# Performance work log

Measured on AMD Instinct MI355X. Metric: run time of the kernel, lower is better.

## Reference

```python
import jax, jax.numpy as jnp
import numpy as np

SEQ, BATCH = 1024, 2
N_HEAD, D_MODEL = 16, 1024
Q_LORA, KV_LORA = 20, 20
ROPE = D_MODEL // N_HEAD // 2   # 32 qk_rope_head_dim
NOPE = D_MODEL // N_HEAD // 2   # 32 qk_nope_head_dim
V_DIM = D_MODEL // N_HEAD       # 64
N_EXP, HID = 4, 1024            # hidden_dim = d_inner//5 = 5120//5
N_GROUP, TOPK_GROUP, TOP_K = 2, 2, 1
ROUTED_SCALE = 1.0


def setup_inputs() -> dict:
    key = jax.random.key(0)
    ks = jax.random.split(key, 16)
    sc = 0.02
    return {
        'dec_inp': jax.random.normal(ks[0], (SEQ, BATCH, D_MODEL), jnp.float32),
        'wq_a': jax.random.normal(ks[1], (D_MODEL, Q_LORA), jnp.float32) * sc,
        'q_norm_w': jnp.ones((Q_LORA,), jnp.float32),
        'wq_b': jax.random.normal(ks[2], (Q_LORA, N_HEAD * (NOPE + ROPE)), jnp.float32) * sc,
        'wkv_a': jax.random.normal(ks[3], (D_MODEL, KV_LORA + ROPE), jnp.float32) * sc,
        'kv_norm_w': jnp.ones((KV_LORA,), jnp.float32),
        'wkv_b': jax.random.normal(ks[4], (KV_LORA, N_HEAD * (NOPE + V_DIM)), jnp.float32) * sc,
        'wo': jax.random.normal(ks[5], (N_HEAD * V_DIM, D_MODEL), jnp.float32) * sc,
        'gate_w': jax.random.normal(ks[6], (N_EXP, D_MODEL), jnp.float32) * sc,
        'exp_gate': jax.random.normal(ks[7], (N_EXP, D_MODEL, HID), jnp.float32) * sc,
        'exp_up': jax.random.normal(ks[8], (N_EXP, D_MODEL, HID), jnp.float32) * sc,
        'exp_down': jax.random.normal(ks[9], (N_EXP, HID, D_MODEL), jnp.float32) * sc,
        'sh_gate': jax.random.normal(ks[10], (D_MODEL, HID), jnp.float32) * sc,
        'sh_up': jax.random.normal(ks[11], (D_MODEL, HID), jnp.float32) * sc,
        'sh_down': jax.random.normal(ks[12], (HID, D_MODEL), jnp.float32) * sc,
    }


def _rms(x, w, eps=1e-6):
    return x * jax.lax.rsqrt(jnp.mean(x * x, axis=-1, keepdims=True) + eps) * w


def _freqs(seqlen):
    # precompute_freqs_cis(rope_dim * n_head, seqlen): dim = 512 here
    dim = ROPE * N_HEAD
    inv = 1.0 / (10000.0 ** (jnp.arange(0, dim, 2, dtype=jnp.float32) / dim))  # [dim//2]
    ang = jnp.arange(seqlen, dtype=jnp.float32)[:, None] * inv[None, :]       # [s, dim//2]
    ang = ang.reshape(seqlen, N_HEAD, ROPE // 2)
    return jnp.cos(ang), jnp.sin(ang)


def _rope(x, cos, sin):
    # x: [b, s, h, ROPE]; interleaved-pair complex rotation
    b, s, h, _ = x.shape
    xr = x.reshape(b, s, h, ROPE // 2, 2)
    x0, x1 = xr[..., 0], xr[..., 1]
    c = cos[None]  # [1, s, h, ROPE//2]
    sn = sin[None]
    o0 = x0 * c - x1 * sn
    o1 = x0 * sn + x1 * c
    return jnp.stack([o0, o1], axis=-1).reshape(b, s, h, ROPE)


def reference(dec_inp, wq_a, q_norm_w, wq_b, wkv_a, kv_norm_w, wkv_b, wo,
              gate_w, exp_gate, exp_up, exp_down, sh_gate, sh_up, sh_down):
    x = jnp.swapaxes(dec_inp, 0, 1)  # [b, s, d]
    b, s, d = x.shape
    # ---- MLA attention ----
    q = _rms(x @ wq_a, q_norm_w) @ wq_b                       # [b, s, h*(nope+rope)]
    q = q.reshape(b, s, N_HEAD, NOPE + ROPE)
    q_nope, q_pe = q[..., :NOPE], q[..., NOPE:]
    kv = x @ wkv_a                                            # [b, s, kv_lora+rope]
    ckv, k_pe = kv[..., :KV_LORA], kv[..., KV_LORA:]
    kvb = (_rms(ckv, kv_norm_w) @ wkv_b).reshape(b, s, N_HEAD, NOPE + V_DIM)
    k_nope, v = kvb[..., :NOPE], kvb[..., NOPE:]
    cos, sin = _freqs(s)
    q_pe = _rope(q_pe, cos, sin)
    k_pe_h = _rope(jnp.broadcast_to(k_pe[:, :, None, :], (b, s, N_HEAD, ROPE)), cos, sin)
    qf = jnp.concatenate([q_nope, q_pe], axis=-1)             # [b, s, h, 64]
    kf = jnp.concatenate([k_nope, k_pe_h], axis=-1)
    scale = 1.0 / np.sqrt(NOPE + ROPE)
    scores = jnp.einsum('bshd,bthd->bhst', qf, kf) * scale    # mask=None in the source forward
    probs = jax.nn.softmax(scores, axis=-1)
    attn = jnp.einsum('bhst,bthd->bshd', probs, v).reshape(b, s, N_HEAD * V_DIM)
    y = attn @ wo                                             # [b, s, d]
    y = jnp.swapaxes(y, 0, 1)                                 # [s, b, d]
    # ---- DeepSeekMoE (group_limited_greedy, top_k=1, 1 shared expert) ----
    xf = y.reshape(-1, d)                                     # [T, d]
    T = xf.shape[0]
    sc = jax.nn.softmax(xf @ gate_w.T, axis=-1)               # [T, E]
    gsc = sc.reshape(T, N_GROUP, N_EXP // N_GROUP).max(axis=-1)  # [T, n_group]
    _, gidx = jax.lax.top_k(gsc, TOPK_GROUP)
    gmask = jax.nn.one_hot(gidx, N_GROUP, dtype=sc.dtype).sum(axis=1)  # [T, n_group]
    smask = jnp.repeat(gmask, N_EXP // N_GROUP, axis=-1)      # [T, E]
    tw, ti = jax.lax.top_k(jnp.where(smask > 0, sc, 0.0), TOP_K)
    comb = (jax.nn.one_hot(ti, N_EXP, dtype=sc.dtype) * tw[..., None]).sum(axis=1) * ROUTED_SCALE  # [T, E]
    g = jnp.einsum('td,edh->teh', xf, exp_gate)
    u = jnp.einsum('td,edh->teh', xf, exp_up)
    dn = jnp.einsum('teh,ehd->ted', jax.nn.silu(g) * u, exp_down)
    routed = jnp.einsum('ted,te->td', dn, comb)
    shared = (jax.nn.silu(xf @ sh_gate) * (xf @ sh_up)) @ sh_down
    return (routed + shared).reshape(s, b, d)
```

## Files before the change

### kernel.cpp

```cpp
#include <hip/hip_runtime.h>
#include <hip/hip_bf16.h>
#include <math.h>

#define SEQ 1024
#define BATCH 2
#define T 2048
#define DM 1024
#define NH 16
#define NOPE 32
#define HD 64
#define QL 20
#define KVL 20
#define KVA 52
#define HID 1024
#define NEXP 4
#define LSTR 80

typedef short bf16x8 __attribute__((ext_vector_type(8)));
typedef float f32x4 __attribute__((ext_vector_type(4)));
typedef float f32x16 __attribute__((ext_vector_type(16)));
typedef __hip_bfloat16 bf16;

static __device__ __forceinline__ float sigmoidf_(float x) {
    return 1.0f / (1.0f + __expf(-x));
}
static __device__ __forceinline__ unsigned short bfbits(float x) {
    bf16 h = __float2bfloat16(x);
    return *reinterpret_cast<unsigned short*>(&h);
}
static __device__ __forceinline__ unsigned cvt_pk_bf16(float lo, float hi) {
    unsigned r;
    asm("v_cvt_pk_bf16_f32 %0, %1, %2" : "=v"(r) : "v"(lo), "v"(hi));
    return r;
}
static __device__ __forceinline__ void gload16(const bf16* g, char* l) {
    __builtin_amdgcn_global_load_lds(
        (const __attribute__((address_space(1))) unsigned int*)g,
        (__attribute__((address_space(3))) unsigned int*)l, 16, 0, 0);
}
static __device__ __forceinline__ void barrier_() {
    asm volatile("" ::: "memory");
    __builtin_amdgcn_s_barrier();
    asm volatile("" ::: "memory");
}
#define VMWAIT(N) asm volatile("s_waitcnt vmcnt(" #N ")" ::: "memory")

__global__ __launch_bounds__(256) void k_setup(
    const float* __restrict__ wo, const float* __restrict__ sg,
    const float* __restrict__ su, const float* __restrict__ sd,
    const float* __restrict__ eg, const float* __restrict__ eu,
    const float* __restrict__ ed,
    bf16* __restrict__ woT, bf16* __restrict__ sgT, bf16* __restrict__ suT,
    bf16* __restrict__ sdT, bf16* __restrict__ egT, bf16* __restrict__ euT,
    bf16* __restrict__ edT,
    const float* __restrict__ wq_a, const float* __restrict__ wkv_a,
    const float* __restrict__ wq_b, const float* __restrict__ wkv_b,
    bf16* __restrict__ loraT, bf16* __restrict__ wqbT, bf16* __restrict__ wkvbT,
    float* __restrict__ ctab, float* __restrict__ stab)
{
    int z = blockIdx.z;
    int tid = threadIdx.x;
    if (z < 16) {
        __shared__ float tile[32][33];
        const float* in; bf16* out;
        if      (z == 0) { in = wo; out = woT; }
        else if (z == 1) { in = sg; out = sgT; }
        else if (z == 2) { in = su; out = suT; }
        else if (z == 3) { in = sd; out = sdT; }
        else if (z < 8)  { size_t o = (size_t)(z - 4)  * DM * HID; in = eg + o; out = egT + o; }
        else if (z < 12) { size_t o = (size_t)(z - 8)  * DM * HID; in = eu + o; out = euT + o; }
        else             { size_t o = (size_t)(z - 12) * HID * DM; in = ed + o; out = edT + o; }
        int c0 = blockIdx.x * 32, r0 = blockIdx.y * 32;
        int tx = tid & 31, ty = tid >> 5;
        #pragma unroll
        for (int ii = 0; ii < 4; ++ii)
            tile[ty + ii * 8][tx] = in[(size_t)(r0 + ty + ii * 8) * 1024 + c0 + tx];
        __syncthreads();
        int c = tid >> 3, rg = (tid & 7) * 4;
        ushort4 o4;
        o4.x = bfbits(tile[rg + 0][c]);
        o4.y = bfbits(tile[rg + 1][c]);
        o4.z = bfbits(tile[rg + 2][c]);
        o4.w = bfbits(tile[rg + 3][c]);
        *(ushort4*)&out[(size_t)(c0 + c) * 1024 + r0 + rg] = o4;
    } else if (z == 16) {
        int s = blockIdx.y * 32 + blockIdx.x;
        int p = tid;
        float freq = exp2f(-(float)p * (13.287712379549449f / 256.0f));
        float ang = (float)s * freq;
        float sn, cs;
        __sincosf(ang, &sn, &cs);
        ctab[s * 256 + p] = cs;
        stab[s * 256 + p] = sn;
    } else {
        int idx = (blockIdx.y * 32 + blockIdx.x) * 256 + tid;
        if (z == 17) {
            if (idx >= 80 * 1024) return;
            int n = idx >> 10, k = idx & 1023;
            float v = (n < 20) ? wq_a[k * QL + n] : (n < 72 ? wkv_a[k * KVA + (n - 20)] : 0.f);
            loraT[idx] = __float2bfloat16(v);
        } else if (z == 18) {
            if (idx >= 1024 * 32) return;
            int n = idx >> 5, k = idx & 31;
            wqbT[idx] = __float2bfloat16(k < 20 ? wq_b[k * DM + n] : 0.f);
        } else {
            if (idx >= 1536 * 32) return;
            int n = idx >> 5, k = idx & 31;
            wkvbT[idx] = __float2bfloat16(k < 20 ? wkv_b[k * (NH * 96) + n] : 0.f);
        }
    }
}

__global__ __launch_bounds__(256) void k_p1(
    const float* __restrict__ dec, const bf16* __restrict__ loraT,
    float* __restrict__ lora4)
{
    __shared__ __align__(16) char As[128 * LSTR];
    __shared__ __align__(16) char Bs[80 * LSTR];
    const int tid = threadIdx.x;
    const int kz = blockIdx.x;
    const int m0 = blockIdx.y * 128;
    const int lane = tid & 63, wave = tid >> 6;
    const int g = lane >> 4, c = lane & 15;
    f32x4 acc[2][5] = {};
    for (int ks = 0; ks < 16; ++ks) {
        int k0 = kz * 512 + ks * 32;
        __syncthreads();
        #pragma unroll
        for (int pass = 0; pass < 4; ++pass) {
            int row = (tid >> 3) + pass * 32;
            int t = m0 + row;
            int b = t >> 10, s = t & 1023;
            f32x4 v = *(const f32x4*)&dec[(size_t)(s * 2 + b) * DM + k0 + (tid & 7) * 4];
            ushort4 h4;
            h4.x = bfbits(v[0]); h4.y = bfbits(v[1]);
            h4.z = bfbits(v[2]); h4.w = bfbits(v[3]);
            *(ushort4*)&As[row * LSTR + (tid & 7) * 8] = h4;
        }
        if (tid < 160) {
            int row = tid >> 1, hf = tid & 1;
            const bf16* src = &loraT[row * 1024 + k0 + hf * 16];
            *(int4*)&Bs[row * LSTR + hf * 32]      = *(const int4*)&src[0];
            *(int4*)&Bs[row * LSTR + hf * 32 + 16] = *(const int4*)&src[8];
        }
        __syncthreads();
        bf16x8 af[2], bff[5];
        #pragma unroll
        for (int mi = 0; mi < 2; ++mi)
            af[mi] = *(const bf16x8*)&As[(wave * 32 + mi * 16 + c) * LSTR + 16 * g];
        #pragma unroll
        for (int nf = 0; nf < 5; ++nf)
            bff[nf] = *(const bf16x8*)&Bs[(nf * 16 + c) * LSTR + 16 * g];
        #pragma unroll
        for (int mi = 0; mi < 2; ++mi)
            #pragma unroll
            for (int nf = 0; nf < 5; ++nf)
                acc[mi][nf] = __builtin_amdgcn_mfma_f32_16x16x32_bf16(af[mi], bff[nf], acc[mi][nf], 0, 0, 0);
    }
    #pragma unroll
    for (int mi = 0; mi < 2; ++mi)
        #pragma unroll
        for (int nf = 0; nf < 5; ++nf)
            #pragma unroll
            for (int r = 0; r < 4; ++r) {
                int col = nf * 16 + c;
                if (col < 72) {
                    int row = m0 + wave * 32 + mi * 16 + 4 * g + r;
                    lora4[((size_t)kz * T + row) * 72 + col] = acc[mi][nf][r];
                }
            }
}

__global__ __launch_bounds__(256) void k_p2(
    const float* __restrict__ lora4, const float* __restrict__ qnw,
    const float* __restrict__ kvnw, bf16* __restrict__ nrmq, bf16* __restrict__ nrmkv,
    int* __restrict__ cnt)
{
    if (blockIdx.x == 0 && threadIdx.x < 16) cnt[threadIdx.x] = 0;
    int t = blockIdx.x * 256 + threadIdx.x;
    float lq[20], lk[20];
    float ssq = 0.f, ssk = 0.f;
    #pragma unroll
    for (int i = 0; i < 20; ++i) {
        lq[i] = lora4[t * 72 + i] + lora4[(size_t)(T + t) * 72 + i];
        ssq += lq[i] * lq[i];
    }
    #pragma unroll
    for (int i = 0; i < 20; ++i) {
        lk[i] = lora4[t * 72 + 20 + i] + lora4[(size_t)(T + t) * 72 + 20 + i];
        ssk += lk[i] * lk[i];
    }
    float fq = rsqrtf(ssq / 20.f + 1e-6f);
    float fk = rsqrtf(ssk / 20.f + 1e-6f);
    #pragma unroll
    for (int i = 0; i < 32; ++i) {
        nrmq[t * 32 + i]  = __float2bfloat16(i < 20 ? lq[i] * fq * qnw[i]  : 0.f);
        nrmkv[t * 32 + i] = __float2bfloat16(i < 20 ? lk[i] * fk * kvnw[i] : 0.f);
    }
}

__global__ __launch_bounds__(256) void k_p2b(
    const float* __restrict__ lora4, const float* __restrict__ ctab,
    const float* __restrict__ stab, bf16* __restrict__ kb)
{
    int t = blockIdx.x, p = threadIdx.x;
    int r = p & 15, h = p >> 4, s = t & (SEQ - 1);
    float y0 = lora4[t * 72 + 40 + 2 * r] + lora4[(size_t)(T + t) * 72 + 40 + 2 * r];
    float y1 = lora4[t * 72 + 41 + 2 * r] + lora4[(size_t)(T + t) * 72 + 41 + 2 * r];
    float cs = ctab[s * 256 + p], sn = stab[s * 256 + p];
    ushort2 pk;
    pk.x = bfbits(y0 * cs - y1 * sn);
    pk.y = bfbits(y0 * sn + y1 * cs);
    *(ushort2*)&kb[(size_t)t * DM + h * HD + NOPE + 2 * r] = pk;
}

__global__ __launch_bounds__(256) void k_p3q(
    const bf16* __restrict__ nrmq, const bf16* __restrict__ wqbT,
    const float* __restrict__ ctab, const float* __restrict__ stab,
    bf16* __restrict__ qb)
{
    __shared__ __align__(16) char As[128 * LSTR];
    __shared__ __align__(16) char Bs[64 * LSTR];
    const int tid = threadIdx.x;
    const int m0 = blockIdx.y * 128, n0 = blockIdx.x * 64;
    const int lane = tid & 63, wave = tid >> 6;
    const int g = lane >> 4, c = lane & 15;
    const int wm = wave >> 1, wn = wave & 1;
    {
        int row = tid >> 1, hf = tid & 1;
        const bf16* sa = &nrmq[(size_t)(m0 + row) * 32 + hf * 16];
        *(int4*)&As[row * LSTR + hf * 32]      = *(const int4*)&sa[0];
        *(int4*)&As[row * LSTR + hf * 32 + 16] = *(const int4*)&sa[8];
        int brow = tid >> 2;
        *(int4*)&Bs[brow * LSTR + (tid & 3) * 16] = *(const int4*)&wqbT[(size_t)(n0 + brow) * 32 + (tid & 3) * 8];
    }
    __syncthreads();
    f32x4 acc[4][2] = {};
    bf16x8 af[4], bfr[2];
    #pragma unroll
    for (int mi = 0; mi < 4; ++mi)
        af[mi] = *(const bf16x8*)&As[(wm * 64 + mi * 16 + c) * LSTR + 16 * g];
    #pragma unroll
    for (int ni = 0; ni < 2; ++ni)
        bfr[ni] = *(const bf16x8*)&Bs[(wn * 32 + ni * 16 + c) * LSTR + 16 * g];
    #pragma unroll
    for (int mi = 0; mi < 4; ++mi)
        #pragma unroll
        for (int ni = 0; ni < 2; ++ni) {
            acc[mi][ni] = __builtin_amdgcn_mfma_f32_16x16x32_bf16(af[mi], bfr[ni], acc[mi][ni], 0, 0, 0);
            #pragma unroll
            for (int r = 0; r < 4; ++r) acc[mi][ni][r] *= 0.18033688f;
        }

    #pragma unroll
    for (int mi = 0; mi < 4; ++mi)
        #pragma unroll
        for (int ni = 0; ni < 2; ++ni) {
            int n = n0 + wn * 32 + ni * 16 + c;
            int w = n & 63;
            if (w < 32) {
                #pragma unroll
                for (int r = 0; r < 4; ++r) {
                    int row = m0 + wm * 64 + mi * 16 + 4 * g + r;
                    qb[(size_t)row * DM + n] = __float2bfloat16(acc[mi][ni][r]);
                }
            } else {
                int h = n >> 6;
                int pidx = h * 16 + ((w - 32) >> 1);
                int odd = w & 1;
                #pragma unroll
                for (int r = 0; r < 4; ++r) {
                    int row = m0 + wm * 64 + mi * 16 + 4 * g + r;
                    int s = row & (SEQ - 1);
                    float own = acc[mi][ni][r];
                    float oth = __shfl_xor(own, 1);
                    float cs = ctab[s * 256 + pidx], sn = stab[s * 256 + pidx];
                    float o = odd ? (oth * sn + own * cs) : (own * cs - oth * sn);
                    qb[(size_t)row * DM + n] = __float2bfloat16(o);
                }
            }
        }
}

__global__ __launch_bounds__(256) void k_p3kv(
    const bf16* __restrict__ nrmkv, const bf16* __restrict__ wkvbT,
    bf16* __restrict__ kb, bf16* __restrict__ vt_g)
{
    __shared__ __align__(16) char As[128 * LSTR];
    __shared__ __align__(16) char Bs[64 * LSTR];
    const int tid = threadIdx.x;
    const int m0 = blockIdx.y * 128, n0 = blockIdx.x * 64;
    const int lane = tid & 63, wave = tid >> 6;
    const int g = lane >> 4, c = lane & 15;
    const int wm = wave >> 1, wn = wave & 1;
    {
        int row = tid >> 1, hf = tid & 1;
        const bf16* sa = &nrmkv[(size_t)(m0 + row) * 32 + hf * 16];
        *(int4*)&As[row * LSTR + hf * 32]      = *(const int4*)&sa[0];
        *(int4*)&As[row * LSTR + hf * 32 + 16] = *(const int4*)&sa[8];
        int brow = tid >> 2;
        *(int4*)&Bs[brow * LSTR + (tid & 3) * 16] = *(const int4*)&wkvbT[(size_t)(n0 + brow) * 32 + (tid & 3) * 8];
    }
    __syncthreads();
    f32x4 acc[4][2] = {};
    bf16x8 af[4], bfr[2];
    #pragma unroll
    for (int mi = 0; mi < 4; ++mi)
        af[mi] = *(const bf16x8*)&As[(wm * 64 + mi * 16 + c) * LSTR + 16 * g];
    #pragma unroll
    for (int ni = 0; ni < 2; ++ni)
        bfr[ni] = *(const bf16x8*)&Bs[(wn * 32 + ni * 16 + c) * LSTR + 16 * g];
    #pragma unroll
    for (int mi = 0; mi < 4; ++mi)
        #pragma unroll
        for (int ni = 0; ni < 2; ++ni)
            acc[mi][ni] = __builtin_amdgcn_mfma_f32_16x16x32_bf16(af[mi], bfr[ni], acc[mi][ni], 0, 0, 0);

    #pragma unroll
    for (int mi = 0; mi < 4; ++mi)
        #pragma unroll
        for (int ni = 0; ni < 2; ++ni) {
            int n = n0 + wn * 32 + ni * 16 + c;
            int h = n / 96, w = n - h * 96;
            int row0 = m0 + wm * 64 + mi * 16 + 4 * g;
            if (w < NOPE) {
                #pragma unroll
                for (int r = 0; r < 4; ++r)
                    kb[(size_t)(row0 + r) * DM + h * HD + w] = __float2bfloat16(acc[mi][ni][r]);
            } else {
                int d = w - NOPE;
                int b = row0 >> 10, s0 = row0 & (SEQ - 1);
                ushort4 v4;
                v4.x = bfbits(acc[mi][ni][0]);
                v4.y = bfbits(acc[mi][ni][1]);
                v4.z = bfbits(acc[mi][ni][2]);
                v4.w = bfbits(acc[mi][ni][3]);
                *(ushort4*)&vt_g[(((size_t)(b * NH + h) * HD + d) << 10) + s0] = v4;
            }
        }
}

__global__ __launch_bounds__(256) void k_attn(
    const bf16* __restrict__ qb, const bf16* __restrict__ kb,
    const bf16* __restrict__ vt_g, bf16* __restrict__ ab)
{
    __shared__ __align__(16) char stage[2][16384];
    __shared__ float pol[2][32][65];
    __shared__ float mll[2][32][2];

    const int qt = blockIdx.x, h = blockIdx.y, b = blockIdx.z;
    const int tid = threadIdx.x;
    const int lane = tid & 63, wave = tid >> 6;
    const int l31 = lane & 31, hi = lane >> 5;
    const int sp = wave >> 1, wq = wave & 1;
    const int q0 = qt * 64 + wq * 32;
    char* ks = stage[sp];
    char* vt = stage[sp] + 8192;
    const int ptid = tid & 127;

    bf16x8 qf[4];
    {
        const bf16* qrow = &qb[(size_t)(b * SEQ + q0 + l31) * DM + h * HD + 8 * hi];
        #pragma unroll
        for (int st = 0; st < 4; ++st)
            qf[st] = *(const bf16x8*)&qrow[16 * st];
    }

    f32x16 o0 = {}, o1 = {};
    float m_run = -3.0e38f, l_run = 0.f;
    const size_t vbase = ((size_t)(b * NH + h) * HD) << 10;

    for (int ktl = 0; ktl < 8; ++ktl) {
        const int kt = sp * 8 + ktl;
        __syncthreads();
        #pragma unroll
        for (int ps = 0; ps < 4; ++ps) {
            int row = (ptid >> 3) + ps * 16;
            int col8 = (ptid & 7) * 8;
            int sw = (col8 * 2) ^ ((row & 7) << 4);
            int4 kv4 = *(const int4*)&kb[(size_t)(b * SEQ + kt * 64 + row) * DM + h * HD + col8];
            *(int4*)&ks[row * 128 + sw] = kv4;
            int4 vv4 = *(const int4*)&vt_g[vbase + ((size_t)row << 10) + kt * 64 + col8];
            *(int4*)&vt[row * 128 + sw] = vv4;
        }
        __syncthreads();

        f32x16 sc0 = {}, sc1 = {};
        #pragma unroll
        for (int st = 0; st < 4; ++st) {
            int colb = 32 * st + 16 * hi;
            int r0 = l31;
            bf16x8 kf0 = *(const bf16x8*)&ks[r0 * 128 + (colb ^ ((r0 & 7) << 4))];
            sc0 = __builtin_amdgcn_mfma_f32_32x32x16_bf16(kf0, qf[st], sc0, 0, 0, 0);
            int r1 = 32 + l31;
            bf16x8 kf1 = *(const bf16x8*)&ks[r1 * 128 + (colb ^ ((r1 & 7) << 4))];
            sc1 = __builtin_amdgcn_mfma_f32_32x32x16_bf16(kf1, qf[st], sc1, 0, 0, 0);
        }

        float mt = fmaxf(sc0[0], sc1[0]);
        #pragma unroll
        for (int i = 1; i < 16; ++i) mt = fmaxf(mt, fmaxf(sc0[i], sc1[i]));
        mt = fmaxf(mt, __shfl_xor(mt, 32));

        if (!__all(mt <= m_run + 8.0f)) {
            float m_new = fmaxf(m_run, mt);
            float corr = exp2f(m_run - m_new);
            m_run = m_new;
            l_run *= corr;
            #pragma unroll
            for (int i = 0; i < 16; ++i) { o0[i] *= corr; o1[i] *= corr; }
        }
        float ls = 0.f;
        #pragma unroll
        for (int i = 0; i < 16; ++i) {
            sc0[i] = exp2f(sc0[i] - m_run);
            sc1[i] = exp2f(sc1[i] - m_run);
            ls += sc0[i] + sc1[i];
        }
        ls += __shfl_xor(ls, 32);
        l_run += ls;

        unsigned pk0[8], pk1[8];
        #pragma unroll
        for (int i = 0; i < 8; ++i) {
            pk0[i] = cvt_pk_bf16(sc0[2 * i], sc0[2 * i + 1]);
            pk1[i] = cvt_pk_bf16(sc1[2 * i], sc1[2 * i + 1]);
        }

#define PV_SUB(PK, KK)                                                          \
        {                                                                       \
            _Pragma("unroll")                                                   \
            for (int s = 0; s < 2; ++s) {                                       \
                unsigned sx = hi ? PK[4*s]   : PK[4*s+2];                       \
                unsigned rx = __shfl_xor(sx, 32);                               \
                unsigned sy = hi ? PK[4*s+1] : PK[4*s+3];                       \
                unsigned ry = __shfl_xor(sy, 32);                               \
                int4 bi;                                                        \
                bi.x = hi ? (int)rx : (int)PK[4*s];                             \
                bi.y = hi ? (int)ry : (int)PK[4*s+1];                           \
                bi.z = hi ? (int)PK[4*s+2] : (int)rx;                           \
                bi.w = hi ? (int)PK[4*s+3] : (int)ry;                           \
                bf16x8 bfr = *(bf16x8*)&bi;                                     \
                int cb = (KK) * 64 + 32 * s + 16 * hi;                          \
                {                                                               \
                    int vr = l31;                                               \
                    bf16x8 vf = *(const bf16x8*)&vt[vr * 128 + (cb ^ ((vr & 7) << 4))]; \
                    o0 = __builtin_amdgcn_mfma_f32_32x32x16_bf16(vf, bfr, o0, 0, 0, 0); \
                }                                                               \
                {                                                               \
                    int vr = 32 + l31;                                          \
                    bf16x8 vf = *(const bf16x8*)&vt[vr * 128 + (cb ^ ((vr & 7) << 4))]; \
                    o1 = __builtin_amdgcn_mfma_f32_32x32x16_bf16(vf, bfr, o1, 0, 0, 0); \
                }                                                               \
            }                                                                   \
        }
        PV_SUB(pk0, 0)
        PV_SUB(pk1, 1)
#undef PV_SUB
    }

    if (sp == 1) {
        #pragma unroll
        for (int i = 0; i < 16; ++i) {
            int d = (i & 3) + 8 * (i >> 2) + 4 * hi;
            pol[wq][l31][d]      = o0[i];
            pol[wq][l31][32 + d] = o1[i];
        }
        if (hi == 0) { mll[wq][l31][0] = m_run; mll[wq][l31][1] = l_run; }
    }
    __syncthreads();
    if (sp == 1) return;

    float m_b = mll[wq][l31][0], l_b = mll[wq][l31][1];
    float M = fmaxf(m_run, m_b);
    float wa = exp2f(m_run - M), wb = exp2f(m_b - M);
    float inv = 1.0f / (l_run * wa + l_b * wb);
    #pragma unroll
    for (int i = 0; i < 16; ++i) {
        int d = (i & 3) + 8 * (i >> 2) + 4 * hi;
        o0[i] = (o0[i] * wa + pol[wq][l31][d]      * wb) * inv;
        o1[i] = (o1[i] * wa + pol[wq][l31][32 + d] * wb) * inv;
    }

    char* tb = stage[wq];
    #pragma unroll
    for (int i = 0; i < 8; ++i) {
        int dbase = 2 * (i & 1) + 8 * (i >> 1) + 4 * hi;
        *(unsigned*)&tb[l31 * 140 + (dbase) * 2]      = cvt_pk_bf16(o0[2 * i], o0[2 * i + 1]);
        *(unsigned*)&tb[l31 * 140 + (32 + dbase) * 2] = cvt_pk_bf16(o1[2 * i], o1[2 * i + 1]);
    }
    __builtin_amdgcn_s_waitcnt(0);
    #pragma unroll
    for (int p = 0; p < 8; ++p) {
        int idx = p * 64 + lane;
        int q = idx >> 4, c8 = idx & 15;
        int2 rv;
        rv.x = *(const int*)&tb[q * 140 + c8 * 8];
        rv.y = *(const int*)&tb[q * 140 + c8 * 8 + 4];
        *(int2*)&ab[(size_t)(b * SEQ + q0 + q) * DM + h * HD + c8 * 4] = rv;
    }
}

__global__ __launch_bounds__(512) void k_mm_plain(
    const bf16* __restrict__ A, const bf16* __restrict__ Bt, bf16* __restrict__ C)
{
    __shared__ __align__(16) char As[2][8192];
    __shared__ __align__(16) char Bs[2][4096];
    const int tid = threadIdx.x;
    const int lane = tid & 63, wave = tid >> 6;
    const int g = lane >> 4, c = lane & 15;
    const int wm = wave >> 1, wn = wave & 1;
    const int m0 = blockIdx.y * 128, n0 = blockIdx.x * 64;

    const int ldr = lane >> 2;
    const int ldc = (lane & 3) * 8;
    const bf16* agp = &A[(size_t)(m0 + wave * 16 + ldr) * DM + ldc];
    const bool doB = wave >= 4;
    const bf16* bgp = &Bt[(size_t)(n0 + (wave & 3) * 16 + ldr) * DM + ldc];
    const int aoffL = wave * 1024, boffL = (wave & 3) * 1024;

    f32x4 acc[2][2] = {};
    const int NT = DM / 32;
    gload16(agp, As[0] + aoffL);
    if (doB) gload16(bgp, Bs[0] + boffL);
    for (int k = 0; k < NT; ++k) {
        const int cur = k & 1;
        if (k + 1 < NT) {
            gload16(agp + (k + 1) * 32, As[cur ^ 1] + aoffL);
            if (doB) gload16(bgp + (k + 1) * 32, Bs[cur ^ 1] + boffL);
            if (doB) VMWAIT(2); else VMWAIT(1);
        } else {
            VMWAIT(0);
        }
        barrier_();
        bf16x8 af[2], bfx[2];
        #pragma unroll
        for (int mi = 0; mi < 2; ++mi)
            af[mi] = *(const bf16x8*)&As[cur][(wm * 32 + mi * 16 + c) * 64 + g * 16];
        #pragma unroll
        for (int ni = 0; ni < 2; ++ni)
            bfx[ni] = *(const bf16x8*)&Bs[cur][(wn * 32 + ni * 16 + c) * 64 + g * 16];
        #pragma unroll
        for (int mi = 0; mi < 2; ++mi)
            #pragma unroll
            for (int ni = 0; ni < 2; ++ni)
                acc[mi][ni] = __builtin_amdgcn_mfma_f32_16x16x32_bf16(af[mi], bfx[ni], acc[mi][ni], 0, 0, 0);
        barrier_();
    }
    #pragma unroll
    for (int mi = 0; mi < 2; ++mi)
        #pragma unroll
        for (int ni = 0; ni < 2; ++ni)
            #pragma unroll
            for (int r = 0; r < 4; ++r)
                C[(size_t)(m0 + wm * 32 + mi * 16 + 4 * g + r) * DM + n0 + wn * 32 + ni * 16 + c]
                    = __float2bfloat16(acc[mi][ni][r]);
}

__global__ __launch_bounds__(512) void k_mm_gu_all(
    const bf16* __restrict__ X, const bf16* __restrict__ egT,
    const bf16* __restrict__ euT, const bf16* __restrict__ sgT,
    const bf16* __restrict__ suT, const int* __restrict__ cnt,
    const int* __restrict__ lists, bf16* __restrict__ act_r,
    bf16* __restrict__ act_s)
{
    const int e = blockIdx.z;
    const bool SH = (e == 4);
    const int ntok = SH ? T : cnt[e];
    const int m0 = blockIdx.y * 128;
    if (m0 >= ntok) return;
    const int n0 = blockIdx.x * 64;
    __shared__ __align__(16) char As[2][8192];
    __shared__ __align__(16) char Bg[2][4096];
    __shared__ __align__(16) char Bu[2][4096];
    __shared__ int rowid[128];
    const int tid = threadIdx.x;
    if (tid < 128) {
        int idx = m0 + tid;
        rowid[tid] = SH ? idx : lists[e * T + (idx < ntok ? idx : ntok - 1)];
    }
    __syncthreads();
    const int lane = tid & 63, wave = tid >> 6;
    const int g = lane >> 4, c = lane & 15;
    const int wm = wave >> 1, wn = wave & 1;
    const bf16* Bge = SH ? sgT : egT + (size_t)e * HID * DM;
    const bf16* Bue = SH ? suT : euT + (size_t)e * HID * DM;
    bf16* act = SH ? act_s : act_r;

    const int ldr = lane >> 2;
    const int ldc = (lane & 3) * 8;
    const int myTok = rowid[wave * 16 + ldr];
    const bf16* agp = &X[(size_t)myTok * DM + ldc];
    const bool isG = wave < 4;
    const bf16* bgp = (isG ? Bge : Bue) + (size_t)(n0 + (wave & 3) * 16 + ldr) * DM + ldc;
    const int aoffL = wave * 1024, boffL = (wave & 3) * 1024;

    f32x4 accg[2][2] = {}, accu[2][2] = {};
    const int NT = DM / 32;
    gload16(agp, As[0] + aoffL);
    gload16(bgp, (isG ? Bg[0] : Bu[0]) + boffL);
    for (int k = 0; k < NT; ++k) {
        const int cur = k & 1;
        if (k + 1 < NT) {
            gload16(agp + (k + 1) * 32, As[cur ^ 1] + aoffL);
            gload16(bgp + (k + 1) * 32, (isG ? Bg[cur ^ 1] : Bu[cur ^ 1]) + boffL);
            VMWAIT(2);
        } else {
            VMWAIT(0);
        }
        barrier_();
        bf16x8 af[2], gf[2], uf[2];
        #pragma unroll
        for (int mi = 0; mi < 2; ++mi)
            af[mi] = *(const bf16x8*)&As[cur][(wm * 32 + mi * 16 + c) * 64 + g * 16];
        #pragma unroll
        for (int ni = 0; ni < 2; ++ni) {
            gf[ni] = *(const bf16x8*)&Bg[cur][(wn * 32 + ni * 16 + c) * 64 + g * 16];
            uf[ni] = *(const bf16x8*)&Bu[cur][(wn * 32 + ni * 16 + c) * 64 + g * 16];
        }
        #pragma unroll
        for (int mi = 0; mi < 2; ++mi)
            #pragma unroll
            for (int ni = 0; ni < 2; ++ni) {
                accg[mi][ni] = __builtin_amdgcn_mfma_f32_16x16x32_bf16(af[mi], gf[ni], accg[mi][ni], 0, 0, 0);
                accu[mi][ni] = __builtin_amdgcn_mfma_f32_16x16x32_bf16(af[mi], uf[ni], accu[mi][ni], 0, 0, 0);
            }
        barrier_();
    }
    #pragma unroll
    for (int mi = 0; mi < 2; ++mi)
        #pragma unroll
        for (int ni = 0; ni < 2; ++ni)
            #pragma unroll
            for (int r = 0; r < 4; ++r) {
                int lr = wm * 32 + mi * 16 + 4 * g + r;
                if (!SH && m0 + lr >= ntok) continue;
                int token = rowid[lr];
                float gv = accg[mi][ni][r], uv = accu[mi][ni][r];
                act[(size_t)token * HID + n0 + wn * 32 + ni * 16 + c] =
                    __float2bfloat16(gv * sigmoidf_(gv) * uv);
            }
}

template<bool ROUTED>
__global__ __launch_bounds__(512) void k_mm_down(
    const bf16* __restrict__ Xact, const bf16* __restrict__ BdT,
    const int* __restrict__ cnt, const int* __restrict__ lists,
    const float* __restrict__ wtok, float* __restrict__ out)
{
    const int e = blockIdx.z;
    const int ntok = ROUTED ? cnt[e] : T;
    const int m0 = blockIdx.y * 128;
    if (m0 >= ntok) return;
    const int n0 = blockIdx.x * 64;
    __shared__ __align__(16) char As[2][8192];
    __shared__ __align__(16) char Bs[2][4096];
    __shared__ int rowid[128];
    const int tid = threadIdx.x;
    if (tid < 128) {
        int idx = m0 + tid;
        rowid[tid] = ROUTED ? lists[e * T + (idx < ntok ? idx : ntok - 1)] : idx;
    }
    __syncthreads();
    const int lane = tid & 63, wave = tid >> 6;
    const int g = lane >> 4, c = lane & 15;
    const int wm = wave >> 1, wn = wave & 1;
    const bf16* Bde = BdT + (ROUTED ? (size_t)e * HID * DM : 0);

    const int ldr = lane >> 2;
    const int ldc = (lane & 3) * 8;
    const int myTok = rowid[wave * 16 + ldr];
    const bf16* agp = &Xact[(size_t)myTok * HID + ldc];
    const bool doB = wave >= 4;
    const bf16* bgp = &Bde[(size_t)(n0 + (wave & 3) * 16 + ldr) * HID + ldc];
    const int aoffL = wave * 1024, boffL = (wave & 3) * 1024;

    f32x4 acc[2][2] = {};
    const int NT = HID / 32;
    gload16(agp, As[0] + aoffL);
    if (doB) gload16(bgp, Bs[0] + boffL);
    for (int k = 0; k < NT; ++k) {
        const int cur = k & 1;
        if (k + 1 < NT) {
            gload16(agp + (k + 1) * 32, As[cur ^ 1] + aoffL);
            if (doB) gload16(bgp + (k + 1) * 32, Bs[cur ^ 1] + boffL);
            if (doB) VMWAIT(2); else VMWAIT(1);
        } else {
            VMWAIT(0);
        }
        barrier_();
        bf16x8 af[2], bfx[2];
        #pragma unroll
        for (int mi = 0; mi < 2; ++mi)
            af[mi] = *(const bf16x8*)&As[cur][(wm * 32 + mi * 16 + c) * 64 + g * 16];
        #pragma unroll
        for (int ni = 0; ni < 2; ++ni)
            bfx[ni] = *(const bf16x8*)&Bs[cur][(wn * 32 + ni * 16 + c) * 64 + g * 16];
        #pragma unroll
        for (int mi = 0; mi < 2; ++mi)
            #pragma unroll
            for (int ni = 0; ni < 2; ++ni)
                acc[mi][ni] = __builtin_amdgcn_mfma_f32_16x16x32_bf16(af[mi], bfx[ni], acc[mi][ni], 0, 0, 0);
        barrier_();
    }
    #pragma unroll
    for (int mi = 0; mi < 2; ++mi)
        #pragma unroll
        for (int ni = 0; ni < 2; ++ni)
            #pragma unroll
            for (int r = 0; r < 4; ++r) {
                int lr = wm * 32 + mi * 16 + 4 * g + r;
                if (ROUTED && m0 + lr >= ntok) continue;
                int token = rowid[lr];
                int bt = token >> 10, st = token & (SEQ - 1);
                size_t oo = (size_t)st * (BATCH * DM) + bt * DM + n0 + wn * 32 + ni * 16 + c;
                if (ROUTED) out[oo] = acc[mi][ni][r] * wtok[token];
                else        out[oo] += acc[mi][ni][r];
            }
}

__global__ __launch_bounds__(256) void k_gate(
    const bf16* __restrict__ y, const float* __restrict__ gw,
    int* __restrict__ cnt, int* __restrict__ lists, float* __restrict__ wtok)
{
    int warp = threadIdx.x >> 6, lane = threadIdx.x & 63;
    int t = blockIdx.x * 4 + warp;
    float acc[NEXP] = {};
    for (int d = lane; d < DM; d += 64) {
        float xv = __bfloat162float(y[(size_t)t * DM + d]);
        #pragma unroll
        for (int e = 0; e < NEXP; ++e) acc[e] += xv * gw[e * DM + d];
    }
    #pragma unroll
    for (int off = 32; off; off >>= 1)
        #pragma unroll
        for (int e = 0; e < NEXP; ++e) acc[e] += __shfl_xor(acc[e], off);
    if (lane == 0) {
        float mx = fmaxf(fmaxf(acc[0], acc[1]), fmaxf(acc[2], acc[3]));
        float ex[NEXP], ssum = 0.f;
        #pragma unroll
        for (int e = 0; e < NEXP; ++e) { ex[e] = __expf(acc[e] - mx); ssum += ex[e]; }
        int best = 0; float bv = ex[0];
        #pragma unroll
        for (int e = 1; e < NEXP; ++e) if (ex[e] > bv) { bv = ex[e]; best = e; }
        wtok[t] = bv / ssum;
        int pos = atomicAdd(&cnt[best], 1);
        lists[best * T + pos] = t;
    }
}

extern "C" void kernel_launch(void* const* d_in, const int* in_sizes, int n_in,
                              void* d_out, int out_size, void* d_ws, size_t ws_size,
                              hipStream_t stream) {
    (void)in_sizes; (void)n_in; (void)out_size; (void)ws_size;
    const float* dec      = (const float*)d_in[0];
    const float* wq_a     = (const float*)d_in[1];
    const float* q_norm_w = (const float*)d_in[2];
    const float* wq_b     = (const float*)d_in[3];
    const float* wkv_a    = (const float*)d_in[4];
    const float* kv_norm_w= (const float*)d_in[5];
    const float* wkv_b    = (const float*)d_in[6];
    const float* wo       = (const float*)d_in[7];
    const float* gate_w   = (const float*)d_in[8];
    const float* exp_gate = (const float*)d_in[9];
    const float* exp_up   = (const float*)d_in[10];
    const float* exp_down = (const float*)d_in[11];
    const float* sh_gate  = (const float*)d_in[12];
    const float* sh_up    = (const float*)d_in[13];
    const float* sh_down  = (const float*)d_in[14];
    float* out = (float*)d_out;

    char* W = (char*)d_ws;
    bf16* qb   = (bf16*)(W);
    bf16* kb   = (bf16*)(W + (4ull  << 20));
    bf16* vt_g = (bf16*)(W + (8ull  << 20));
    char* SMALL = W + (12ull << 20);
    bf16* ab   = (bf16*)(W + (12ull << 20));
    bf16* woT = (bf16*)(W + (16ull << 20));
    bf16* sgT = (bf16*)(W + (18ull << 20));
    bf16* suT = (bf16*)(W + (20ull << 20));
    bf16* sdT = (bf16*)(W + (22ull << 20));
    bf16* egT = (bf16*)(W + (24ull << 20));
    bf16* euT = (bf16*)(W + (32ull << 20));
    bf16* edT = (bf16*)(W + (40ull << 20));
    int*   cnt   = (int*)(W + (48ull << 20));
    int*   lists = cnt + 16;
    float* wtok  = (float*)(lists + NEXP * T);
    bf16* yb    = qb;
    bf16* act_r = kb;
    bf16* act_s = vt_g;

    float* lora4 = (float*)(SMALL);
    bf16*  loraT = (bf16*) (SMALL + 1179648);
    bf16*  wqbT  = (bf16*) (SMALL + 1343488);
    bf16*  wkvbT = (bf16*) (SMALL + 1409024);
    bf16*  nrmq  = (bf16*) (SMALL + 1507328);
    bf16*  nrmkv = (bf16*) (SMALL + 1638400);
    float* ctab  = (float*)(SMALL + 1769472);
    float* stab  = (float*)(SMALL + 2818048);

    k_setup<<<dim3(32, 32, 20), 256, 0, stream>>>(
        wo, sh_gate, sh_up, sh_down, exp_gate, exp_up, exp_down,
        woT, sgT, suT, sdT, egT, euT, edT,
        wq_a, wkv_a, wq_b, wkv_b, loraT, wqbT, wkvbT, ctab, stab);

    k_p1<<<dim3(2, 16), 256, 0, stream>>>(dec, loraT, lora4);
    k_p2<<<T / 256, 256, 0, stream>>>(lora4, q_norm_w, kv_norm_w, nrmq, nrmkv, cnt);
    k_p2b<<<T, 256, 0, stream>>>(lora4, ctab, stab, kb);
    k_p3q<<<dim3(16, 16), 256, 0, stream>>>(nrmq, wqbT, ctab, stab, qb);
    k_p3kv<<<dim3(24, 16), 256, 0, stream>>>(nrmkv, wkvbT, kb, vt_g);

    k_attn<<<dim3(SEQ / 64, NH, BATCH), 256, 0, stream>>>(qb, kb, vt_g, ab);
    k_mm_plain<<<dim3(DM / 64, T / 128), 512, 0, stream>>>(ab, woT, yb);
    k_gate<<<T / 4, 256, 0, stream>>>(yb, gate_w, cnt, lists, wtok);
    k_mm_gu_all<<<dim3(HID / 64, T / 128, NEXP + 1), 512, 0, stream>>>(
        yb, egT, euT, sgT, suT, cnt, lists, act_r, act_s);
    k_mm_down<true><<<dim3(DM / 64, T / 128, NEXP), 512, 0, stream>>>(act_r, edT, cnt, lists, wtok, out);
    k_mm_down<false><<<dim3(DM / 64, T / 128, 1), 512, 0, stream>>>(act_s, sdT, cnt, lists, wtok, out);
}
```

Measured before the change: 193.3 us.

## Merge prologue kernels, widen attention blocks, fuse shared and routed down projections

Merges the norm and k-rope kernels into one launch, and the q and kv up-projection kernels into one grid split along z. Attention blocks go to 512 threads covering 128 queries with four query waves per key split, which halves the K staging loop per thread. The shared-expert down projection is fused into the routed down kernel: each token's routed and shared outputs are summed in a single store, removing a separate launch and a read-modify-write pass over the output. Costs are more shared memory and registers in the fused down kernel and fewer attention blocks in the grid.

After: 183.9 us. 1.05x faster.

```diff
diff --git a/kernel.cpp b/kernel.cpp
--- a/kernel.cpp
+++ b/kernel.cpp
@@ -171,54 +171,57 @@
             }
 }
 
-__global__ __launch_bounds__(256) void k_p2(
+__global__ __launch_bounds__(256) void k_p2m(
     const float* __restrict__ lora4, const float* __restrict__ qnw,
-    const float* __restrict__ kvnw, bf16* __restrict__ nrmq, bf16* __restrict__ nrmkv,
-    int* __restrict__ cnt)
+    const float* __restrict__ kvnw, const float* __restrict__ ctab,
+    const float* __restrict__ stab, bf16* __restrict__ nrmq,
+    bf16* __restrict__ nrmkv, bf16* __restrict__ kb, int* __restrict__ cnt)
 {
-    if (blockIdx.x == 0 && threadIdx.x < 16) cnt[threadIdx.x] = 0;
-    int t = blockIdx.x * 256 + threadIdx.x;
-    float lq[20], lk[20];
-    float ssq = 0.f, ssk = 0.f;
-    #pragma unroll
-    for (int i = 0; i < 20; ++i) {
-        lq[i] = lora4[t * 72 + i] + lora4[(size_t)(T + t) * 72 + i];
-        ssq += lq[i] * lq[i];
-    }
-    #pragma unroll
-    for (int i = 0; i < 20; ++i) {
-        lk[i] = lora4[t * 72 + 20 + i] + lora4[(size_t)(T + t) * 72 + 20 + i];
-        ssk += lk[i] * lk[i];
-    }
-    float fq = rsqrtf(ssq / 20.f + 1e-6f);
-    float fk = rsqrtf(ssk / 20.f + 1e-6f);
-    #pragma unroll
-    for (int i = 0; i < 32; ++i) {
-        nrmq[t * 32 + i]  = __float2bfloat16(i < 20 ? lq[i] * fq * qnw[i]  : 0.f);
-        nrmkv[t * 32 + i] = __float2bfloat16(i < 20 ? lk[i] * fk * kvnw[i] : 0.f);
-    }
-}
-
-__global__ __launch_bounds__(256) void k_p2b(
-    const float* __restrict__ lora4, const float* __restrict__ ctab,
-    const float* __restrict__ stab, bf16* __restrict__ kb)
+    int bid = blockIdx.x, tid = threadIdx.x;
+    if (bid == 0 && tid < 16) cnt[tid] = 0;
+    {
+        int t = bid, p = tid;
+        int r = p & 15, h = p >> 4, s = t & (SEQ - 1);
+        float y0 = lora4[t * 72 + 40 + 2 * r] + lora4[(size_t)(T + t) * 72 + 40 + 2 * r];
+        float y1 = lora4[t * 72 + 41 + 2 * r] + lora4[(size_t)(T + t) * 72 + 41 + 2 * r];
+        float cs = ctab[s * 256 + p], sn = stab[s * 256 + p];
+        ushort2 pk;
+        pk.x = bfbits(y0 * cs - y1 * sn);
+        pk.y = bfbits(y0 * sn + y1 * cs);
+        *(ushort2*)&kb[(size_t)t * DM + h * HD + NOPE + 2 * r] = pk;
+    }
+    if (bid < 8) {
+        int t = bid * 256 + tid;
+        float lq[20], lk[20];
+        float ssq = 0.f, ssk = 0.f;
+        #pragma unroll
+        for (int i = 0; i < 20; ++i) {
+            lq[i] = lora4[t * 72 + i] + lora4[(size_t)(T + t) * 72 + i];
+            ssq += lq[i] * lq[i];
+        }
+        #pragma unroll
+        for (int i = 0; i < 20; ++i) {
+            lk[i] = lora4[t * 72 + 20 + i] + lora4[(size_t)(T + t) * 72 + 20 + i];
+            ssk += lk[i] * lk[i];
+        }
+        float fq = rsqrtf(ssq / 20.f + 1e-6f);
+        float fk = rsqrtf(ssk / 20.f + 1e-6f);
+        #pragma unroll
+        for (int i = 0; i < 32; ++i) {
+            nrmq[t * 32 + i]  = __float2bfloat16(i < 20 ? lq[i] * fq * qnw[i]  : 0.f);
+            nrmkv[t * 32 + i] = __float2bfloat16(i < 20 ? lk[i] * fk * kvnw[i] : 0.f);
+        }
+    }
+}
+
+__global__ __launch_bounds__(256) void k_p3(
+    const bf16* __restrict__ nrmq, const bf16* __restrict__ wqbT,
+    const bf16* __restrict__ nrmkv, const bf16* __restrict__ wkvbT,
+    const float* __restrict__ ctab, const float* __restrict__ stab,
+    bf16* __restrict__ qb, bf16* __restrict__ kb, bf16* __restrict__ vt_g)
 {
-    int t = blockIdx.x, p = threadIdx.x;
-    int r = p & 15, h = p >> 4, s = t & (SEQ - 1);
-    float y0 = lora4[t * 72 + 40 + 2 * r] + lora4[(size_t)(T + t) * 72 + 40 + 2 * r];
-    float y1 = lora4[t * 72 + 41 + 2 * r] + lora4[(size_t)(T + t) * 72 + 41 + 2 * r];
-    float cs = ctab[s * 256 + p], sn = stab[s * 256 + p];
-    ushort2 pk;
-    pk.x = bfbits(y0 * cs - y1 * sn);
-    pk.y = bfbits(y0 * sn + y1 * cs);
-    *(ushort2*)&kb[(size_t)t * DM + h * HD + NOPE + 2 * r] = pk;
-}
-
-__global__ __launch_bounds__(256) void k_p3q(
-    const bf16* __restrict__ nrmq, const bf16* __restrict__ wqbT,
-    const float* __restrict__ ctab, const float* __restrict__ stab,
-    bf16* __restrict__ qb)
-{
+    const int zq = (blockIdx.z == 0);
+    if (zq && blockIdx.x >= 16) return;
     __shared__ __align__(16) char As[128 * LSTR];
     __shared__ __align__(16) char Bs[64 * LSTR];
     const int tid = threadIdx.x;
@@ -226,13 +229,15 @@
     const int lane = tid & 63, wave = tid >> 6;
     const int g = lane >> 4, c = lane & 15;
     const int wm = wave >> 1, wn = wave & 1;
+    const bf16* nrm = zq ? nrmq : nrmkv;
+    const bf16* wT  = zq ? wqbT : wkvbT;
     {
         int row = tid >> 1, hf = tid & 1;
-        const bf16* sa = &nrmq[(size_t)(m0 + row) * 32 + hf * 16];
+        const bf16* sa = &nrm[(size_t)(m0 + row) * 32 + hf * 16];
         *(int4*)&As[row * LSTR + hf * 32]      = *(const int4*)&sa[0];
         *(int4*)&As[row * LSTR + hf * 32 + 16] = *(const int4*)&sa[8];
         int brow = tid >> 2;
-        *(int4*)&Bs[brow * LSTR + (tid & 3) * 16] = *(const int4*)&wqbT[(size_t)(n0 + brow) * 32 + (tid & 3) * 8];
+        *(int4*)&Bs[brow * LSTR + (tid & 3) * 16] = *(const int4*)&wT[(size_t)(n0 + brow) * 32 + (tid & 3) * 8];
     }
     __syncthreads();
     f32x4 acc[4][2] = {};
@@ -246,117 +251,83 @@
     #pragma unroll
     for (int mi = 0; mi < 4; ++mi)
         #pragma unroll
-        for (int ni = 0; ni < 2; ++ni) {
+        for (int ni = 0; ni < 2; ++ni)
             acc[mi][ni] = __builtin_amdgcn_mfma_f32_16x16x32_bf16(af[mi], bfr[ni], acc[mi][ni], 0, 0, 0);
-            #pragma unroll
-            for (int r = 0; r < 4; ++r) acc[mi][ni][r] *= 0.18033688f;
-        }
-
-    #pragma unroll
-    for (int mi = 0; mi < 4; ++mi)
-        #pragma unroll
-        for (int ni = 0; ni < 2; ++ni) {
-            int n = n0 + wn * 32 + ni * 16 + c;
-            int w = n & 63;
-            if (w < 32) {
+
+    if (zq) {
+        #pragma unroll
+        for (int mi = 0; mi < 4; ++mi)
+            #pragma unroll
+            for (int ni = 0; ni < 2; ++ni) {
                 #pragma unroll
-                for (int r = 0; r < 4; ++r) {
-                    int row = m0 + wm * 64 + mi * 16 + 4 * g + r;
-                    qb[(size_t)row * DM + n] = __float2bfloat16(acc[mi][ni][r]);
-                }
-            } else {
-                int h = n >> 6;
-                int pidx = h * 16 + ((w - 32) >> 1);
-                int odd = w & 1;
-                #pragma unroll
-                for (int r = 0; r < 4; ++r) {
-                    int row = m0 + wm * 64 + mi * 16 + 4 * g + r;
-                    int s = row & (SEQ - 1);
-                    float own = acc[mi][ni][r];
-                    float oth = __shfl_xor(own, 1);
-                    float cs = ctab[s * 256 + pidx], sn = stab[s * 256 + pidx];
-                    float o = odd ? (oth * sn + own * cs) : (own * cs - oth * sn);
-                    qb[(size_t)row * DM + n] = __float2bfloat16(o);
+                for (int r = 0; r < 4; ++r) acc[mi][ni][r] *= 0.18033688f;
+                int n = n0 + wn * 32 + ni * 16 + c;
+                int w = n & 63;
+                if (w < 32) {
+                    #pragma unroll
+                    for (int r = 0; r < 4; ++r) {
+                        int row = m0 + wm * 64 + mi * 16 + 4 * g + r;
+                        qb[(size_t)row * DM + n] = __float2bfloat16(acc[mi][ni][r]);
+                    }
+                } else {
+                    int h = n >> 6;
+                    int pidx = h * 16 + ((w - 32) >> 1);
+                    int odd = w & 1;
+                    #pragma unroll
+                    for (int r = 0; r < 4; ++r) {
+                        int row = m0 + wm * 64 + mi * 16 + 4 * g + r;
+                        int s = row & (SEQ - 1);
+                        float own = acc[mi][ni][r];
+                        float oth = __shfl_xor(own, 1);
+                        float cs = ctab[s * 256 + pidx], sn = stab[s * 256 + pidx];
+                        float o = odd ? (oth * sn + own * cs) : (own * cs - oth * sn);
+                        qb[(size_t)row * DM + n] = __float2bfloat16(o);
+                    }
                 }
             }
-        }
-}
-
-__global__ __launch_bounds__(256) void k_p3kv(
-    const bf16* __restrict__ nrmkv, const bf16* __restrict__ wkvbT,
-    bf16* __restrict__ kb, bf16* __restrict__ vt_g)
-{
-    __shared__ __align__(16) char As[128 * LSTR];
-    __shared__ __align__(16) char Bs[64 * LSTR];
-    const int tid = threadIdx.x;
-    const int m0 = blockIdx.y * 128, n0 = blockIdx.x * 64;
-    const int lane = tid & 63, wave = tid >> 6;
-    const int g = lane >> 4, c = lane & 15;
-    const int wm = wave >> 1, wn = wave & 1;
-    {
-        int row = tid >> 1, hf = tid & 1;
-        const bf16* sa = &nrmkv[(size_t)(m0 + row) * 32 + hf * 16];
-        *(int4*)&As[row * LSTR + hf * 32]      = *(const int4*)&sa[0];
-        *(int4*)&As[row * LSTR + hf * 32 + 16] = *(const int4*)&sa[8];
-        int brow = tid >> 2;
-        *(int4*)&Bs[brow * LSTR + (tid & 3) * 16] = *(const int4*)&wkvbT[(size_t)(n0 + brow) * 32 + (tid & 3) * 8];
-    }
-    __syncthreads();
-    f32x4 acc[4][2] = {};
-    bf16x8 af[4], bfr[2];
-    #pragma unroll
-    for (int mi = 0; mi < 4; ++mi)
-        af[mi] = *(const bf16x8*)&As[(wm * 64 + mi * 16 + c) * LSTR + 16 * g];
-    #pragma unroll
-    for (int ni = 0; ni < 2; ++ni)
-        bfr[ni] = *(const bf16x8*)&Bs[(wn * 32 + ni * 16 + c) * LSTR + 16 * g];
-    #pragma unroll
-    for (int mi = 0; mi < 4; ++mi)
-        #pragma unroll
-        for (int ni = 0; ni < 2; ++ni)
-            acc[mi][ni] = __builtin_amdgcn_mfma_f32_16x16x32_bf16(af[mi], bfr[ni], acc[mi][ni], 0, 0, 0);
-
-    #pragma unroll
-    for (int mi = 0; mi < 4; ++mi)
-        #pragma unroll
-        for (int ni = 0; ni < 2; ++ni) {
-            int n = n0 + wn * 32 + ni * 16 + c;
-            int h = n / 96, w = n - h * 96;
-            int row0 = m0 + wm * 64 + mi * 16 + 4 * g;
-            if (w < NOPE) {
-                #pragma unroll
-                for (int r = 0; r < 4; ++r)
-                    kb[(size_t)(row0 + r) * DM + h * HD + w] = __float2bfloat16(acc[mi][ni][r]);
-            } else {
-                int d = w - NOPE;
-                int b = row0 >> 10, s0 = row0 & (SEQ - 1);
-                ushort4 v4;
-                v4.x = bfbits(acc[mi][ni][0]);
-                v4.y = bfbits(acc[mi][ni][1]);
-                v4.z = bfbits(acc[mi][ni][2]);
-                v4.w = bfbits(acc[mi][ni][3]);
-                *(ushort4*)&vt_g[(((size_t)(b * NH + h) * HD + d) << 10) + s0] = v4;
+    } else {
+        #pragma unroll
+        for (int mi = 0; mi < 4; ++mi)
+            #pragma unroll
+            for (int ni = 0; ni < 2; ++ni) {
+                int n = n0 + wn * 32 + ni * 16 + c;
+                int h = n / 96, w = n - h * 96;
+                int row0 = m0 + wm * 64 + mi * 16 + 4 * g;
+                if (w < NOPE) {
+                    #pragma unroll
+                    for (int r = 0; r < 4; ++r)
+                        kb[(size_t)(row0 + r) * DM + h * HD + w] = __float2bfloat16(acc[mi][ni][r]);
+                } else {
+                    int d = w - NOPE;
+                    int b = row0 >> 10, s0 = row0 & (SEQ - 1);
+                    ushort4 v4;
+                    v4.x = bfbits(acc[mi][ni][0]);
+                    v4.y = bfbits(acc[mi][ni][1]);
+                    v4.z = bfbits(acc[mi][ni][2]);
+                    v4.w = bfbits(acc[mi][ni][3]);
+                    *(ushort4*)&vt_g[(((size_t)(b * NH + h) * HD + d) << 10) + s0] = v4;
+                }
             }
-        }
-}
-
-__global__ __launch_bounds__(256) void k_attn(
+    }
+}
+
+__global__ __launch_bounds__(512) void k_attn(
     const bf16* __restrict__ qb, const bf16* __restrict__ kb,
     const bf16* __restrict__ vt_g, bf16* __restrict__ ab)
 {
     __shared__ __align__(16) char stage[2][16384];
-    __shared__ float pol[2][32][65];
-    __shared__ float mll[2][32][2];
+    __shared__ float pol[4][32][65];
+    __shared__ float mll[4][32][2];
 
     const int qt = blockIdx.x, h = blockIdx.y, b = blockIdx.z;
     const int tid = threadIdx.x;
     const int lane = tid & 63, wave = tid >> 6;
     const int l31 = lane & 31, hi = lane >> 5;
-    const int sp = wave >> 1, wq = wave & 1;
-    const int q0 = qt * 64 + wq * 32;
+    const int sp = wave >> 2, wq = wave & 3;
+    const int q0 = qt * 128 + wq * 32;
     char* ks = stage[sp];
     char* vt = stage[sp] + 8192;
-    const int ptid = tid & 127;
+    const int ptid = tid & 255;
 
     bf16x8 qf[4];
     {
@@ -374,8 +345,8 @@
         const int kt = sp * 8 + ktl;
         __syncthreads();
         #pragma unroll
-        for (int ps = 0; ps < 4; ++ps) {
-            int row = (ptid >> 3) + ps * 16;
+        for (int ps = 0; ps < 2; ++ps) {
+            int row = (ptid >> 3) + ps * 32;
             int col8 = (ptid & 7) * 8;
             int sw = (col8 * 2) ^ ((row & 7) << 4);
             int4 kv4 = *(const int4*)&kb[(size_t)(b * SEQ + kt * 64 + row) * DM + h * HD + col8];
@@ -482,7 +453,7 @@
         o1[i] = (o1[i] * wa + pol[wq][l31][32 + d] * wb) * inv;
     }
 
-    char* tb = stage[wq];
+    char* tb = stage[0] + wq * 8192;
     #pragma unroll
     for (int i = 0; i < 8; ++i) {
         int dbase = 2 * (i & 1) + 8 * (i >> 1) + 4 * hi;
@@ -642,65 +613,76 @@
             }
 }
 
-template<bool ROUTED>
-__global__ __launch_bounds__(512) void k_mm_down(
-    const bf16* __restrict__ Xact, const bf16* __restrict__ BdT,
+__global__ __launch_bounds__(512) void k_mm_down_f(
+    const bf16* __restrict__ Xr, const bf16* __restrict__ Xs,
+    const bf16* __restrict__ edT, const bf16* __restrict__ sdT,
     const int* __restrict__ cnt, const int* __restrict__ lists,
     const float* __restrict__ wtok, float* __restrict__ out)
 {
     const int e = blockIdx.z;
-    const int ntok = ROUTED ? cnt[e] : T;
+    const int ntok = cnt[e];
     const int m0 = blockIdx.y * 128;
     if (m0 >= ntok) return;
     const int n0 = blockIdx.x * 64;
-    __shared__ __align__(16) char As[2][8192];
-    __shared__ __align__(16) char Bs[2][4096];
+    __shared__ __align__(16) char Ar[2][8192];
+    __shared__ __align__(16) char Az[2][8192];
+    __shared__ __align__(16) char Br[2][4096];
+    __shared__ __align__(16) char Bz[2][4096];
     __shared__ int rowid[128];
     const int tid = threadIdx.x;
     if (tid < 128) {
         int idx = m0 + tid;
-        rowid[tid] = ROUTED ? lists[e * T + (idx < ntok ? idx : ntok - 1)] : idx;
+        rowid[tid] = lists[e * T + (idx < ntok ? idx : ntok - 1)];
     }
     __syncthreads();
     const int lane = tid & 63, wave = tid >> 6;
     const int g = lane >> 4, c = lane & 15;
     const int wm = wave >> 1, wn = wave & 1;
-    const bf16* Bde = BdT + (ROUTED ? (size_t)e * HID * DM : 0);
+    const bf16* Bde = edT + (size_t)e * HID * DM;
 
     const int ldr = lane >> 2;
     const int ldc = (lane & 3) * 8;
     const int myTok = rowid[wave * 16 + ldr];
-    const bf16* agp = &Xact[(size_t)myTok * HID + ldc];
-    const bool doB = wave >= 4;
-    const bf16* bgp = &Bde[(size_t)(n0 + (wave & 3) * 16 + ldr) * HID + ldc];
+    const bf16* agr = &Xr[(size_t)myTok * HID + ldc];
+    const bf16* ags = &Xs[(size_t)myTok * HID + ldc];
+    const bool isR = wave < 4;
+    const bf16* bgp = (isR ? Bde : sdT) + (size_t)(n0 + (wave & 3) * 16 + ldr) * HID + ldc;
     const int aoffL = wave * 1024, boffL = (wave & 3) * 1024;
 
-    f32x4 acc[2][2] = {};
+    f32x4 accr[2][2] = {}, accs[2][2] = {};
     const int NT = HID / 32;
-    gload16(agp, As[0] + aoffL);
-    if (doB) gload16(bgp, Bs[0] + boffL);
+    gload16(agr, Ar[0] + aoffL);
+    gload16(ags, Az[0] + aoffL);
+    gload16(bgp, (isR ? Br[0] : Bz[0]) + boffL);
     for (int k = 0; k < NT; ++k) {
         const int cur = k & 1;
         if (k + 1 < NT) {
-            gload16(agp + (k + 1) * 32, As[cur ^ 1] + aoffL);
-            if (doB) gload16(bgp + (k + 1) * 32, Bs[cur ^ 1] + boffL);
-            if (doB) VMWAIT(2); else VMWAIT(1);
+            gload16(agr + (k + 1) * 32, Ar[cur ^ 1] + aoffL);
+            gload16(ags + (k + 1) * 32, Az[cur ^ 1] + aoffL);
+            gload16(bgp + (k + 1) * 32, (isR ? Br[cur ^ 1] : Bz[cur ^ 1]) + boffL);
+            VMWAIT(3);
         } else {
             VMWAIT(0);
         }
         barrier_();
-        bf16x8 af[2], bfx[2];
+        bf16x8 afr[2], afs[2], bfr[2], bfs[2];
+        #pragma unroll
+        for (int mi = 0; mi < 2; ++mi) {
+            afr[mi] = *(const bf16x8*)&Ar[cur][(wm * 32 + mi * 16 + c) * 64 + g * 16];
+            afs[mi] = *(const bf16x8*)&Az[cur][(wm * 32 + mi * 16 + c) * 64 + g * 16];
+        }
+        #pragma unroll
+        for (int ni = 0; ni < 2; ++ni) {
+            bfr[ni] = *(const bf16x8*)&Br[cur][(wn * 32 + ni * 16 + c) * 64 + g * 16];
+            bfs[ni] = *(const bf16x8*)&Bz[cur][(wn * 32 + ni * 16 + c) * 64 + g * 16];
+        }
         #pragma unroll
         for (int mi = 0; mi < 2; ++mi)
-            af[mi] = *(const bf16x8*)&As[cur][(wm * 32 + mi * 16 + c) * 64 + g * 16];
-        #pragma unroll
-        for (int ni = 0; ni < 2; ++ni)
-            bfx[ni] = *(const bf16x8*)&Bs[cur][(wn * 32 + ni * 16 + c) * 64 + g * 16];
-        #pragma unroll
-        for (int mi = 0; mi < 2; ++mi)
-            #pragma unroll
-            for (int ni = 0; ni < 2; ++ni)
-                acc[mi][ni] = __builtin_amdgcn_mfma_f32_16x16x32_bf16(af[mi], bfx[ni], acc[mi][ni], 0, 0, 0);
+            #pragma unroll
+            for (int ni = 0; ni < 2; ++ni) {
+                accr[mi][ni] = __builtin_amdgcn_mfma_f32_16x16x32_bf16(afr[mi], bfr[ni], accr[mi][ni], 0, 0, 0);
+                accs[mi][ni] = __builtin_amdgcn_mfma_f32_16x16x32_bf16(afs[mi], bfs[ni], accs[mi][ni], 0, 0, 0);
+            }
         barrier_();
     }
     #pragma unroll
@@ -710,12 +692,11 @@
             #pragma unroll
             for (int r = 0; r < 4; ++r) {
                 int lr = wm * 32 + mi * 16 + 4 * g + r;
-                if (ROUTED && m0 + lr >= ntok) continue;
+                if (m0 + lr >= ntok) continue;
                 int token = rowid[lr];
                 int bt = token >> 10, st = token & (SEQ - 1);
                 size_t oo = (size_t)st * (BATCH * DM) + bt * DM + n0 + wn * 32 + ni * 16 + c;
-                if (ROUTED) out[oo] = acc[mi][ni][r] * wtok[token];
-                else        out[oo] += acc[mi][ni][r];
+                out[oo] = accr[mi][ni][r] * wtok[token] + accs[mi][ni][r];
             }
 }
 
@@ -805,16 +786,16 @@
         wq_a, wkv_a, wq_b, wkv_b, loraT, wqbT, wkvbT, ctab, stab);
 
     k_p1<<<dim3(2, 16), 256, 0, stream>>>(dec, loraT, lora4);
-    k_p2<<<T / 256, 256, 0, stream>>>(lora4, q_norm_w, kv_norm_w, nrmq, nrmkv, cnt);
-    k_p2b<<<T, 256, 0, stream>>>(lora4, ctab, stab, kb);
-    k_p3q<<<dim3(16, 16), 256, 0, stream>>>(nrmq, wqbT, ctab, stab, qb);
-    k_p3kv<<<dim3(24, 16), 256, 0, stream>>>(nrmkv, wkvbT, kb, vt_g);
-
-    k_attn<<<dim3(SEQ / 64, NH, BATCH), 256, 0, stream>>>(qb, kb, vt_g, ab);
+    k_p2m<<<T, 256, 0, stream>>>(lora4, q_norm_w, kv_norm_w, ctab, stab,
+                                 nrmq, nrmkv, kb, cnt);
+    k_p3<<<dim3(24, 16, 2), 256, 0, stream>>>(nrmq, wqbT, nrmkv, wkvbT,
+                                              ctab, stab, qb, kb, vt_g);
+
+    k_attn<<<dim3(SEQ / 128, NH, BATCH), 512, 0, stream>>>(qb, kb, vt_g, ab);
     k_mm_plain<<<dim3(DM / 64, T / 128), 512, 0, stream>>>(ab, woT, yb);
     k_gate<<<T / 4, 256, 0, stream>>>(yb, gate_w, cnt, lists, wtok);
     k_mm_gu_all<<<dim3(HID / 64, T / 128, NEXP + 1), 512, 0, stream>>>(
         yb, egT, euT, sgT, suT, cnt, lists, act_r, act_s);
-    k_mm_down<true><<<dim3(DM / 64, T / 128, NEXP), 512, 0, stream>>>(act_r, edT, cnt, lists, wtok, out);
-    k_mm_down<false><<<dim3(DM / 64, T / 128, 1), 512, 0, stream>>>(act_s, sdT, cnt, lists, wtok, out);
-}
+    k_mm_down_f<<<dim3(DM / 64, T / 128, NEXP), 512, 0, stream>>>(
+        act_r, act_s, edT, sdT, cnt, lists, wtok, out);
+}
```
